# Optimization experiments

Hardware: AMD Instinct MI355X
Metric: run time of the kernel (lower is better)

The kernel has to match this reference:

```python
import jax, jax.numpy as jnp
import numpy as np

N, IN_FEATS, OUT_FEATS = 8192, 512, 256


def setup_inputs() -> dict:
    key = jax.random.key(0)
    k1, k2, k3, k4 = jax.random.split(key, 4)
    feature_mat = jax.random.normal(k1, (N, IN_FEATS), dtype=jnp.float32)
    # Xavier-uniform style init for W and W2
    limW = float(np.sqrt(6.0 / (IN_FEATS + OUT_FEATS)))
    W = jax.random.uniform(k2, (IN_FEATS, OUT_FEATS), minval=-limW, maxval=limW, dtype=jnp.float32)
    limW2 = float(np.sqrt(6.0 / (2 * OUT_FEATS + 1)))
    W2 = jax.random.uniform(k3, (2 * OUT_FEATS, 1), minval=-limW2, maxval=limW2, dtype=jnp.float32)
    adj_mat = jax.random.randint(k4, (N, N), 0, 2, dtype=jnp.int32)
    return {"feature_mat": feature_mat, "W": W, "W2": W2, "adj_mat": adj_mat}


def reference(feature_mat, W, W2, adj_mat):
    out_feats = W.shape[1]
    Wh = feature_mat @ W                      # [N, F']
    Wh1 = Wh @ W2[:out_feats, :]              # [N, 1]
    Wh2 = Wh @ W2[out_feats:, :]              # [N, 1]
    e = Wh1 + Wh2.T                           # [N, N] broadcast add
    e = jnp.where(e > 0, e, 0.2 * e)          # leaky_relu(0.2)
    # NOTE: original masks with ZERO (not -inf) before softmax — faithful.
    e = jnp.where(adj_mat > 0, e, jnp.zeros((), dtype=e.dtype))
    attention = jax.nn.softmax(e, axis=1)     # row softmax over all N
    h_prime = attention @ Wh                  # [N, F']
    return jax.nn.relu(h_prime)
```

## Files before the change

kernel.cpp:

```cpp
#include <hip/hip_runtime.h>
#include <hip/hip_bf16.h>
#include <cstdint>
#include <cstddef>

#define NR 8192
#define FOUT 256
#define KIN 512
#define KSPLIT 4
#define JCHUNK (NR / KSPLIT)
#define BKJ 64
#define NSTEP (JCHUNK / BKJ)
#define IROWS 128

typedef __attribute__((ext_vector_type(8))) short bf16x8;
typedef __attribute__((ext_vector_type(4))) float f32x4;

__device__ __forceinline__ unsigned f2bf(float x) {
  unsigned u = __float_as_uint(x);
  u += 0x7fffu + ((u >> 16) & 1u);
  return u >> 16;
}
__device__ __forceinline__ unsigned f2bf_n(float x) {
  __hip_bfloat16 b = __float2bfloat16(x);
  unsigned short us;
  __builtin_memcpy(&us, &b, 2);
  return (unsigned)us;
}
__device__ __forceinline__ float bf2f_n(unsigned h) {
  unsigned short us = (unsigned short)h;
  __hip_bfloat16 b;
  __builtin_memcpy(&b, &us, 2);
  return __bfloat162float(b);
}
__device__ __forceinline__ unsigned fkey(float x) {
  unsigned u = __float_as_uint(x);
  return (u & 0x80000000u) ? ~u : (u | 0x80000000u);
}
__device__ __forceinline__ float fkey_dec(unsigned k) {
  return __uint_as_float((k & 0x80000000u) ? (k ^ 0x80000000u) : ~k);
}

#define GLDS(g, l)                                                            \
  __builtin_amdgcn_global_load_lds(                                           \
      (const __attribute__((address_space(1))) unsigned int*)(g),             \
      (__attribute__((address_space(3))) unsigned int*)(l), 16, 0, 0)

__global__ __launch_bounds__(256) void k0_prep(const float* __restrict__ W,
                                               const float* __restrict__ W2,
                                               float* __restrict__ w1,
                                               float* __restrict__ w2,
                                               char* __restrict__ WTbf,
                                               unsigned* __restrict__ maxkey) {
  if (blockIdx.x == 0 && threadIdx.x == 0) *maxkey = 0u;
  int wv = threadIdx.x >> 6, lane = threadIdx.x & 63;
  int k = blockIdx.x * 4 + wv;
  int f4 = lane * 4;
  float4 wr = *(const float4*)(W + (size_t)k * FOUT + f4);
  float4 a = *(const float4*)(W2 + f4);
  float4 b = *(const float4*)(W2 + FOUT + f4);
  float d1 = wr.x * a.x + wr.y * a.y + wr.z * a.z + wr.w * a.w;
  float d2 = wr.x * b.x + wr.y * b.y + wr.z * b.z + wr.w * b.w;
#pragma unroll
  for (int off = 32; off; off >>= 1) {
    d1 += __shfl_xor(d1, off);
    d2 += __shfl_xor(d2, off);
  }
  if (lane == 0) {
    w1[k] = d1;
    w2[k] = d2;
  }
  int kt = k >> 5, kl = k & 31;
  float wv4[4] = {wr.x, wr.y, wr.z, wr.w};
#pragma unroll
  for (int ff = 0; ff < 4; ++ff) {
    int f = f4 + ff;
    size_t addr = (size_t)kt * 16384 + (f >> 4) * 1024 +
                  (((f & 15) | (((kl >> 3) & 3) << 4)) * 16) + (kl & 7) * 2;
    *(unsigned short*)(WTbf + addr) = (unsigned short)f2bf(wv4[ff]);
  }
}

__global__ __launch_bounds__(256) void k2_fused(
    const float* __restrict__ X, const char* __restrict__ WTbf,
    const float* __restrict__ w1, const float* __restrict__ w2,
    char* __restrict__ WhTf, float* __restrict__ Wh1, float* __restrict__ Wh2,
    unsigned* __restrict__ maxkey) {
  __shared__ char smem[2 * 18432 + 4096];
  char* buf0 = smem;
  char* buf1 = smem + 18432;
  char* wlds = smem + 2 * 18432;
  int t = threadIdx.x, wv = t >> 6, lane = t & 63;
  int jb = blockIdx.x * 32;
  int jr = t >> 3, koff = (t & 7) * 4;
  int cA = (jr & 15) | (((koff >> 3) & 3) << 4);
  int swA = cA ^ (((cA >> 4) & 3) << 2);
  int aoff = (jr >> 4) * 1024 + swA * 16 + ((koff & 4) << 1);
  int slotR = lane ^ (((lane >> 4) & 3) << 2);
  const float* xrow = X + (size_t)(jb + jr) * KIN + koff;

  {
    float2 a_ = *(const float2*)(w1 + t * 2);
    float2 b_ = *(const float2*)(w2 + t * 2);
    *(float2*)(wlds + t * 8) = a_;
    *(float2*)(wlds + 2048 + t * 8) = b_;
  }
  __syncthreads();

  float4 st0, st1, st2, st3;
  float d1 = 0.f, d2 = 0.f;
  f32x4 acc[2][4];
#pragma unroll
  for (int a = 0; a < 2; ++a)
#pragma unroll
    for (int b = 0; b < 4; ++b) acc[a][b] = (f32x4){0.f, 0.f, 0.f, 0.f};

#define K2_GLB(KT, BUFW)                                                      \
  do {                                                                        \
    const char* gs_ = WTbf + ((size_t)(KT) << 14) + (wv << 12) + lane * 16;   \
    char* ld_ = (BUFW) + 2048 + (wv << 12);                                   \
    GLDS(gs_, ld_);                                                           \
    GLDS(gs_ + 1024, ld_ + 1024);                                             \
    GLDS(gs_ + 2048, ld_ + 2048);                                             \
    GLDS(gs_ + 3072, ld_ + 3072);                                             \
  } while (0)

#define K2_LDX(KT, ST) (ST) = *(const float4*)(xrow + (KT) * 32)

#define K2_AGEN(ST, BUFW, SNUM)                                               \
  do {                                                                        \
    uint2 a_;                                                                 \
    a_.x = f2bf((ST).x) | (f2bf((ST).y) << 16);                               \
    a_.y = f2bf((ST).z) | (f2bf((ST).w) << 16);                               \
    *(uint2*)((BUFW) + aoff) = a_;                                            \
    float4 wa_ = *(const float4*)(wlds + ((SNUM)*32 + koff) * 4);             \
    float4 wb_ = *(const float4*)(wlds + 2048 + ((SNUM)*32 + koff) * 4);      \
    d1 += (ST).x * wa_.x + (ST).y * wa_.y + (ST).z * wa_.z + (ST).w * wa_.w;  \
    d2 += (ST).x * wb_.x + (ST).y * wb_.y + (ST).z * wb_.z + (ST).w * wb_.w;  \
  } while (0)

#define K2_ITER(S, BUFR, BUFW, STC, STF)                                      \
  do {                                                                        \
    int s_ = (S);                                                             \
    if (s_ + 1 < 16) K2_GLB(s_ + 1, BUFW);                                    \
    K2_LDX((s_ + 3 < 16) ? s_ + 3 : 15, STF);                                 \
    if (s_ + 1 < 16) K2_AGEN(STC, BUFW, s_ + 1);                              \
    bf16x8 a0 = *(const bf16x8*)((BUFR) + slotR * 16);                        \
    bf16x8 a1 = *(const bf16x8*)((BUFR) + 1024 + slotR * 16);                 \
    bf16x8 b0 = *(const bf16x8*)((BUFR) + 2048 + (wv * 4 + 0) * 1024 + lane * 16); \
    bf16x8 b1 = *(const bf16x8*)((BUFR) + 2048 + (wv * 4 + 1) * 1024 + lane * 16); \
    bf16x8 b2 = *(const bf16x8*)((BUFR) + 2048 + (wv * 4 + 2) * 1024 + lane * 16); \
    bf16x8 b3 = *(const bf16x8*)((BUFR) + 2048 + (wv * 4 + 3) * 1024 + lane * 16); \
    acc[0][0] = __builtin_amdgcn_mfma_f32_16x16x32_bf16(a0, b0, acc[0][0], 0, 0, 0); \
    acc[0][1] = __builtin_amdgcn_mfma_f32_16x16x32_bf16(a0, b1, acc[0][1], 0, 0, 0); \
    acc[0][2] = __builtin_amdgcn_mfma_f32_16x16x32_bf16(a0, b2, acc[0][2], 0, 0, 0); \
    acc[0][3] = __builtin_amdgcn_mfma_f32_16x16x32_bf16(a0, b3, acc[0][3], 0, 0, 0); \
    acc[1][0] = __builtin_amdgcn_mfma_f32_16x16x32_bf16(a1, b0, acc[1][0], 0, 0, 0); \
    acc[1][1] = __builtin_amdgcn_mfma_f32_16x16x32_bf16(a1, b1, acc[1][1], 0, 0, 0); \
    acc[1][2] = __builtin_amdgcn_mfma_f32_16x16x32_bf16(a1, b2, acc[1][2], 0, 0, 0); \
    acc[1][3] = __builtin_amdgcn_mfma_f32_16x16x32_bf16(a1, b3, acc[1][3], 0, 0, 0); \
    __builtin_amdgcn_sched_barrier(0);                                        \
    asm volatile("s_waitcnt vmcnt(1)");                                       \
    asm volatile("s_waitcnt lgkmcnt(0)");                                     \
    __builtin_amdgcn_s_barrier();                                             \
    __builtin_amdgcn_sched_barrier(0);                                        \
  } while (0)

  K2_GLB(0, buf0);
  K2_LDX(0, st0);
  K2_LDX(1, st1);
  K2_LDX(2, st2);
  K2_AGEN(st0, buf0, 0);
  __builtin_amdgcn_sched_barrier(0);
  asm volatile("s_waitcnt vmcnt(2)");
  asm volatile("s_waitcnt lgkmcnt(0)");
  __builtin_amdgcn_s_barrier();
  __builtin_amdgcn_sched_barrier(0);

  for (int s4 = 0; s4 < 16; s4 += 4) {
    K2_ITER(s4 + 0, buf0, buf1, st1, st3);
    K2_ITER(s4 + 1, buf1, buf0, st2, st0);
    K2_ITER(s4 + 2, buf0, buf1, st3, st1);
    K2_ITER(s4 + 3, buf1, buf0, st0, st2);
  }
#undef K2_ITER
#undef K2_AGEN
#undef K2_LDX
#undef K2_GLB

  int q = lane >> 4;
#pragma unroll
  for (int mi = 0; mi < 2; ++mi)
#pragma unroll
    for (int nn = 0; nn < 4; ++nn) {
      int u2 = wv * 4 + nn;
      int cell = (lane & 15) | ((((mi * 2) + (q >> 1)) & 3) << 4);
      uint2 v;
      v.x = f2bf(acc[mi][nn].x) | (f2bf(acc[mi][nn].y) << 16);
      v.y = f2bf(acc[mi][nn].z) | (f2bf(acc[mi][nn].w) << 16);
      *(uint2*)(buf0 + 2048 + u2 * 1024 + cell * 16 + ((q & 1) << 3)) = v;
    }
  __syncthreads();
  char* wb = WhTf + (size_t)blockIdx.x * 16384;
#pragma unroll
  for (int q2 = 0; q2 < 4; ++q2) {
    uint4 v = *(const uint4*)(buf0 + 2048 + q2 * 4096 + t * 16);
    *(uint4*)(wb + q2 * 4096 + t * 16) = v;
  }

  d1 += __shfl_xor(d1, 1);
  d1 += __shfl_xor(d1, 2);
  d1 += __shfl_xor(d1, 4);
  d2 += __shfl_xor(d2, 1);
  d2 += __shfl_xor(d2, 2);
  d2 += __shfl_xor(d2, 4);
  if ((t & 7) == 0) {
    Wh1[jb + jr] = d1;
    Wh2[jb + jr] = d2;
  }
  float mx = d2;
#pragma unroll
  for (int off = 32; off >= 8; off >>= 1) mx = fmaxf(mx, __shfl_xor(mx, off));
  __shared__ float red[4];
  if (lane == 0) red[wv] = mx;
  __syncthreads();
  if (t == 0) {
    float bm = fmaxf(fmaxf(red[0], red[1]), fmaxf(red[2], red[3]));
    atomicMax(maxkey, fkey(bm));
  }
}

__device__ __forceinline__ uint2 hv4(int4 aq, float4 wq, float wh1, float m,
                                     float enm, float& z) {
  float s0 = wh1 + wq.x, s1 = wh1 + wq.y, s2 = wh1 + wq.z, s3 = wh1 + wq.w;
  s0 = fmaxf(s0, 0.2f * s0);
  s1 = fmaxf(s1, 0.2f * s1);
  s2 = fmaxf(s2, 0.2f * s2);
  s3 = fmaxf(s3, 0.2f * s3);
  float w0 = aq.x > 0 ? __expf(s0 - m) : enm;
  float w1 = aq.y > 0 ? __expf(s1 - m) : enm;
  float w2 = aq.z > 0 ? __expf(s2 - m) : enm;
  float w3 = aq.w > 0 ? __expf(s3 - m) : enm;
  unsigned h0 = f2bf_n(w0), h1 = f2bf_n(w1), h2 = f2bf_n(w2), h3 = f2bf_n(w3);
  z += bf2f_n(h0) + bf2f_n(h1) + bf2f_n(h2) + bf2f_n(h3);
  uint2 r;
  r.x = h0 | (h1 << 16);
  r.y = h2 | (h3 << 16);
  return r;
}
__device__ __forceinline__ uint4 hv8(int4 a0, int4 a1, float4 w0, float4 w1,
                                     float wh1, float m, float enm, float& z) {
  uint2 r0 = hv4(a0, w0, wh1, m, enm, z);
  uint2 r1 = hv4(a1, w1, wh1, m, enm, z);
  return (uint4){r0.x, r0.y, r1.x, r1.y};
}

__global__ __launch_bounds__(1024, 4) void k3_attn(
    const int* __restrict__ adj, const char* __restrict__ WhTf,
    const float* __restrict__ Wh1, const float* __restrict__ Wh2,
    const unsigned* __restrict__ maxptr, float* __restrict__ PVp,
    float* __restrict__ Zp) {
  __shared__ char smem[40960];
  char* abuf0 = smem;
  char* abuf1 = smem + 16384;
  char* wlds = smem + 32768;
  int t = threadIdx.x, wv = t >> 6, lane = t & 63;
  int kc = blockIdx.x & 3;
  int ib = blockIdx.x >> 2;
  int ibase = ib * IROWS;
  int jbch = kc * JCHUNK;
  int r0 = t >> 3;
  int j8 = (t & 7) * 8;
  int iglob = ibase + r0;
  float maxwh2 = fkey_dec(*maxptr);
  float wh1 = Wh1[iglob];
  float m = fmaxf(0.f, wh1 + maxwh2);
  float enm = __expf(-m);
  int unitA = (r0 >> 4) * 2 + (j8 >> 5);
  int cA = (r0 & 15) | (((j8 & 31) >> 3) << 4);
  int swA = cA ^ (((cA >> 4) & 3) << 2);
  int aoff = unitA * 1024 + swA * 16;
  int slotR = lane ^ (((lane >> 4) & 3) << 2);
  const int* adjrow = adj + ((size_t)iglob << 13) + jbch + j8;
  int g = wv >> 1, h = wv & 1;
  const char* bbase = WhTf + ((size_t)(kc * 64) << 14) + (size_t)(2 * g) * 1024 +
                      (size_t)lane * 16;
  const char* wl = wlds + j8 * 4;

  *(float2*)(wlds + t * 8) = *(const float2*)(Wh2 + jbch + t * 2);
  __syncthreads();

  bf16x8 bA00, bA01, bA10, bA11, bB00, bB01, bB10, bB11;
  int4 st0_a, st0_b, st1_a, st1_b;
  f32x4 acc[4][2];
#pragma unroll
  for (int a = 0; a < 4; ++a)
#pragma unroll
    for (int b = 0; b < 2; ++b) acc[a][b] = (f32x4){0.f, 0.f, 0.f, 0.f};
  float zacc = 0.f;

#define K3_LDB(S, B00, B01, B10, B11)                                         \
  do {                                                                        \
    int sc_ = (S) < NSTEP ? (S) : NSTEP - 1;                                  \
    const char* bp_ = bbase + (size_t)(2 * sc_) * 16384;                      \
    B00 = *(const bf16x8*)(bp_);                                 \
    B01 = *(const bf16x8*)(bp_ + 16384);                         \
    B10 = *(const bf16x8*)(bp_ + 1024);                          \
    B11 = *(const bf16x8*)(bp_ + 16384 + 1024);                  \
  } while (0)

#define K3_LDA(S, ST)                                                         \
  do {                                                                        \
    int sc_ = (S) < NSTEP ? (S) : NSTEP - 1;                                  \
    ST##_a = *(const int4*)(adjrow + sc_ * BKJ);                              \
    ST##_b = *(const int4*)(adjrow + sc_ * BKJ + 4);                          \
  } while (0)

#define K3_HV(S, AW, STC)                                                     \
  do {                                                                        \
    float4 wq0_ = *(const float4*)(wl + ((S) + 1) * 256);                     \
    float4 wq1_ = *(const float4*)(wl + ((S) + 1) * 256 + 16);                \
    uint4 a_ = hv8(STC##_a, STC##_b, wq0_, wq1_, wh1, m, enm, zacc);          \
    *(uint4*)((AW) + aoff) = a_;                                              \
  } while (0)

#define K3_MFMA(AR, BC00, BC01, BC10, BC11)                                   \
  do {                                                                        \
    _Pragma("unroll")                                                         \
    for (int rf_ = 0; rf_ < 4; ++rf_) {                                       \
      int ub_ = (h * 4 + rf_) * 2;                                            \
      bf16x8 a0_ = *(const bf16x8*)((AR) + (ub_ + 0) * 1024 + slotR * 16);    \
      bf16x8 a1_ = *(const bf16x8*)((AR) + (ub_ + 1) * 1024 + slotR * 16);    \
      acc[rf_][0] = __builtin_amdgcn_mfma_f32_16x16x32_bf16(a0_, BC00, acc[rf_][0], 0, 0, 0); \
      acc[rf_][1] = __builtin_amdgcn_mfma_f32_16x16x32_bf16(a0_, BC10, acc[rf_][1], 0, 0, 0); \
      acc[rf_][0] = __builtin_amdgcn_mfma_f32_16x16x32_bf16(a1_, BC01, acc[rf_][0], 0, 0, 0); \
      acc[rf_][1] = __builtin_amdgcn_mfma_f32_16x16x32_bf16(a1_, BC11, acc[rf_][1], 0, 0, 0); \
    }                                                                         \
  } while (0)

#define K3_TAIL                                                               \
  do {                                                                        \
    __builtin_amdgcn_sched_barrier(0);                                        \
    asm volatile("s_waitcnt lgkmcnt(0)" ::: "memory");                        \
    __builtin_amdgcn_s_barrier();                                             \
    __builtin_amdgcn_sched_barrier(0);                                        \
  } while (0)

#define K3_ITER_H(S, AR, AW, BC00, BC01, BC10, BC11, BF00, BF01, BF10, BF11,  \
                  STC, DO_HV)                                                 \
  do {                                                                        \
    int s_ = (S);                                                             \
    K3_LDB(s_ + 1, BF00, BF01, BF10, BF11);                                   \
    if (DO_HV) K3_HV(s_, AW, STC);                                            \
    K3_LDA(s_ + 3, STC);                                                      \
    K3_MFMA(AR, BC00, BC01, BC10, BC11);                                      \
    K3_TAIL;                                                                  \
  } while (0)

#define K3_ITER_M(S, AR, AW, BC00, BC01, BC10, BC11, BF00, BF01, BF10, BF11,  \
                  STC, DO_HV)                                                 \
  do {                                                                        \
    int s_ = (S);                                                             \
    K3_LDB(s_ + 1, BF00, BF01, BF10, BF11);                                   \
    K3_MFMA(AR, BC00, BC01, BC10, BC11);                                      \
    if (DO_HV) K3_HV(s_, AW, STC);                                            \
    K3_LDA(s_ + 3, STC);                                                      \
    K3_TAIL;                                                                  \
  } while (0)

  K3_LDB(0, bA00, bA01, bA10, bA11);
  int4 adj0a = *(const int4*)(adjrow);
  int4 adj0b = *(const int4*)(adjrow + 4);
  K3_LDA(1, st1);
  K3_LDA(2, st0);
  {
    float4 wq0 = *(const float4*)(wl);
    float4 wq1 = *(const float4*)(wl + 16);
    uint4 a0 = hv8(adj0a, adj0b, wq0, wq1, wh1, m, enm, zacc);
    *(uint4*)(abuf0 + aoff) = a0;
  }
  K3_TAIL;

  if ((wv & 1) == 0) {
    for (int s2 = 0; s2 < NSTEP - 2; s2 += 2) {
      K3_ITER_H(s2 + 0, abuf0, abuf1, bA00, bA01, bA10, bA11, bB00, bB01,
                bB10, bB11, st1, 1);
      K3_ITER_H(s2 + 1, abuf1, abuf0, bB00, bB01, bB10, bB11, bA00, bA01,
                bA10, bA11, st0, 1);
    }
    K3_ITER_H(NSTEP - 2, abuf0, abuf1, bA00, bA01, bA10, bA11, bB00, bB01,
              bB10, bB11, st1, 1);
    K3_ITER_H(NSTEP - 1, abuf1, abuf0, bB00, bB01, bB10, bB11, bA00, bA01,
              bA10, bA11, st0, 0);
  } else {
    for (int s2 = 0; s2 < NSTEP - 2; s2 += 2) {
      K3_ITER_M(s2 + 0, abuf0, abuf1, bA00, bA01, bA10, bA11, bB00, bB01,
                bB10, bB11, st1, 1);
      K3_ITER_M(s2 + 1, abuf1, abuf0, bB00, bB01, bB10, bB11, bA00, bA01,
                bA10, bA11, st0, 1);
    }
    K3_ITER_M(NSTEP - 2, abuf0, abuf1, bA00, bA01, bA10, bA11, bB00, bB01,
              bB10, bB11, st1, 1);
    K3_ITER_M(NSTEP - 1, abuf1, abuf0, bB00, bB01, bB10, bB11, bA00, bA01,
              bA10, bA11, st0, 0);
  }
#undef K3_ITER_H
#undef K3_ITER_M
#undef K3_TAIL
#undef K3_MFMA
#undef K3_HV
#undef K3_LDA
#undef K3_LDB

  zacc += __shfl_xor(zacc, 1);
  zacc += __shfl_xor(zacc, 2);
  zacc += __shfl_xor(zacc, 4);
  if ((t & 7) == 0) Zp[(size_t)kc * NR + iglob] = zacc;
#pragma unroll
  for (int rf = 0; rf < 4; ++rf)
#pragma unroll
    for (int un = 0; un < 2; ++un) {
      int f = (2 * g + un) * 16 + (lane & 15);
      int row0 = ibase + (h * 4 + rf) * 16 + ((lane >> 4) << 2);
      size_t base = ((size_t)kc * NR + row0) * FOUT + f;
      PVp[base + 0 * FOUT] = acc[rf][un].x;
      PVp[base + 1 * FOUT] = acc[rf][un].y;
      PVp[base + 2 * FOUT] = acc[rf][un].z;
      PVp[base + 3 * FOUT] = acc[rf][un].w;
    }
}

__global__ __launch_bounds__(256) void k4_reduce(const float* __restrict__ PVp,
                                                 const float* __restrict__ Zp,
                                                 float* __restrict__ out) {
  int tid = blockIdx.x * 256 + threadIdx.x;
  int i = tid >> 6;
  int f4 = (tid & 63) * 4;
  float z = Zp[i] + Zp[NR + i] + Zp[2 * NR + i] + Zp[3 * NR + i];
  float4 a = {0.f, 0.f, 0.f, 0.f};
#pragma unroll
  for (int c = 0; c < KSPLIT; ++c) {
    float4 p = *(const float4*)(PVp + ((size_t)c * NR + i) * FOUT + f4);
    a.x += p.x;
    a.y += p.y;
    a.z += p.z;
    a.w += p.w;
  }
  float inv = 1.f / z;
  float4 r;
  r.x = fmaxf(a.x * inv, 0.f);
  r.y = fmaxf(a.y * inv, 0.f);
  r.z = fmaxf(a.z * inv, 0.f);
  r.w = fmaxf(a.w * inv, 0.f);
  *(float4*)(out + (size_t)i * FOUT + f4) = r;
}

extern "C" void kernel_launch(void* const* d_in, const int* in_sizes, int n_in,
                              void* d_out, int out_size, void* d_ws,
                              size_t ws_size, hipStream_t stream) {
  const float* X = (const float*)d_in[0];
  const float* W = (const float*)d_in[1];
  const float* W2 = (const float*)d_in[2];
  const int* adj = (const int*)d_in[3];
  float* out = (float*)d_out;
  char* ws = (char*)d_ws;

  const size_t WHT_OFF = 0;
  const size_t WTBF_OFF = (size_t)4 * 1024 * 1024;
  const size_t W1_OFF = WTBF_OFF + 256 * 1024;
  const size_t W2V_OFF = W1_OFF + 2048;
  const size_t WH1_OFF = W2V_OFF + 2048;
  const size_t WH2_OFF = WH1_OFF + 32768;
  const size_t MXK_OFF = WH2_OFF + 32768;
  const size_t ZP_OFF = MXK_OFF + 256;
  const size_t PV_OFF = ZP_OFF + (size_t)KSPLIT * NR * 4;

  char* WhTf = ws + WHT_OFF;
  char* WTbf = ws + WTBF_OFF;
  float* w1 = (float*)(ws + W1_OFF);
  float* w2 = (float*)(ws + W2V_OFF);
  float* Wh1 = (float*)(ws + WH1_OFF);
  float* Wh2 = (float*)(ws + WH2_OFF);
  unsigned* maxkey = (unsigned*)(ws + MXK_OFF);
  float* Zp = (float*)(ws + ZP_OFF);
  float* PVp = (float*)(ws + PV_OFF);

  k0_prep<<<128, 256, 0, stream>>>(W, W2, w1, w2, WTbf, maxkey);
  k2_fused<<<256, 256, 0, stream>>>(X, WTbf, w1, w2, WhTf, Wh1, Wh2, maxkey);
  k3_attn<<<256, 1024, 0, stream>>>(adj, WhTf, Wh1, Wh2, maxkey, PVp, Zp);
  k4_reduce<<<2048, 256, 0, stream>>>(PVp, Zp, out);
}
```

Measured before the change: 106.9 us.

## Process two K-steps per barrier window with four rotating LDS attention buffers

```diff
diff --git a/kernel.cpp b/kernel.cpp
--- a/kernel.cpp
+++ b/kernel.cpp
@@ -259,10 +259,9 @@
     const float* __restrict__ Wh1, const float* __restrict__ Wh2,
     const unsigned* __restrict__ maxptr, float* __restrict__ PVp,
     float* __restrict__ Zp) {
-  __shared__ char smem[40960];
-  char* abuf0 = smem;
-  char* abuf1 = smem + 16384;
-  char* wlds = smem + 32768;
+  __shared__ char smem[73728];
+  char* ab[4] = {smem, smem + 16384, smem + 32768, smem + 49152};
+  char* wlds = smem + 65536;
   int t = threadIdx.x, wv = t >> 6, lane = t & 63;
   int kc = blockIdx.x & 3;
   int ib = blockIdx.x >> 2;
@@ -289,8 +288,8 @@
   *(float2*)(wlds + t * 8) = *(const float2*)(Wh2 + jbch + t * 2);
   __syncthreads();
 
-  bf16x8 bA00, bA01, bA10, bA11, bB00, bB01, bB10, bB11;
-  int4 st0_a, st0_b, st1_a, st1_b;
+  bf16x8 p00, p01, p10, p11, q00, q01, q10, q11;
+  int4 stC_a, stC_b, stD_a, stD_b;
   f32x4 acc[4][2];
 #pragma unroll
   for (int a = 0; a < 4; ++a)
@@ -315,11 +314,11 @@
     ST##_b = *(const int4*)(adjrow + sc_ * BKJ + 4);                          \
   } while (0)
 
-#define K3_HV(S, AW, STC)                                                     \
-  do {                                                                        \
-    float4 wq0_ = *(const float4*)(wl + ((S) + 1) * 256);                     \
-    float4 wq1_ = *(const float4*)(wl + ((S) + 1) * 256 + 16);                \
-    uint4 a_ = hv8(STC##_a, STC##_b, wq0_, wq1_, wh1, m, enm, zacc);          \
+#define K3_HVG(SS, AW, ST)                                                    \
+  do {                                                                        \
+    float4 wq0_ = *(const float4*)(wl + (SS) * 256);                          \
+    float4 wq1_ = *(const float4*)(wl + (SS) * 256 + 16);                     \
+    uint4 a_ = hv8(ST##_a, ST##_b, wq0_, wq1_, wh1, m, enm, zacc);            \
     *(uint4*)((AW) + aoff) = a_;                                              \
   } while (0)
 
@@ -345,69 +344,74 @@
     __builtin_amdgcn_sched_barrier(0);                                        \
   } while (0)
 
-#define K3_ITER_H(S, AR, AW, BC00, BC01, BC10, BC11, BF00, BF01, BF10, BF11,  \
-                  STC, DO_HV)                                                 \
-  do {                                                                        \
-    int s_ = (S);                                                             \
-    K3_LDB(s_ + 1, BF00, BF01, BF10, BF11);                                   \
-    if (DO_HV) K3_HV(s_, AW, STC);                                            \
-    K3_LDA(s_ + 3, STC);                                                      \
-    K3_MFMA(AR, BC00, BC01, BC10, BC11);                                      \
+#define K3_WIN_H(S, PR0, PR1, PW0, PW1, DO_HV)                                \
+  do {                                                                        \
+    K3_LDB((S), p00, p01, p10, p11);                                          \
+    K3_LDB((S) + 1, q00, q01, q10, q11);                                      \
+    if (DO_HV) {                                                              \
+      K3_HVG((S) + 2, PW0, stC);                                              \
+      K3_HVG((S) + 3, PW1, stD);                                              \
+    }                                                                         \
+    K3_LDA((S) + 4, stC);                                                     \
+    K3_LDA((S) + 5, stD);                                                     \
+    K3_MFMA(PR0, p00, p01, p10, p11);                                         \
+    K3_MFMA(PR1, q00, q01, q10, q11);                                         \
     K3_TAIL;                                                                  \
   } while (0)
 
-#define K3_ITER_M(S, AR, AW, BC00, BC01, BC10, BC11, BF00, BF01, BF10, BF11,  \
-                  STC, DO_HV)                                                 \
-  do {                                                                        \
-    int s_ = (S);                                                             \
-    K3_LDB(s_ + 1, BF00, BF01, BF10, BF11);                                   \
-    K3_MFMA(AR, BC00, BC01, BC10, BC11);                                      \
-    if (DO_HV) K3_HV(s_, AW, STC);                                            \
-    K3_LDA(s_ + 3, STC);                                                      \
+#define K3_WIN_M(S, PR0, PR1, PW0, PW1, DO_HV)                                \
+  do {                                                                        \
+    K3_LDB((S), p00, p01, p10, p11);                                          \
+    K3_LDB((S) + 1, q00, q01, q10, q11);                                      \
+    K3_MFMA(PR0, p00, p01, p10, p11);                                         \
+    K3_MFMA(PR1, q00, q01, q10, q11);                                         \
+    if (DO_HV) {                                                              \
+      K3_HVG((S) + 2, PW0, stC);                                              \
+      K3_HVG((S) + 3, PW1, stD);                                              \
+    }                                                                         \
+    K3_LDA((S) + 4, stC);                                                     \
+    K3_LDA((S) + 5, stD);                                                     \
     K3_TAIL;                                                                  \
   } while (0)
 
-  K3_LDB(0, bA00, bA01, bA10, bA11);
-  int4 adj0a = *(const int4*)(adjrow);
-  int4 adj0b = *(const int4*)(adjrow + 4);
-  K3_LDA(1, st1);
-  K3_LDA(2, st0);
   {
+    int4 a0a = *(const int4*)(adjrow);
+    int4 a0b = *(const int4*)(adjrow + 4);
+    int4 a1a = *(const int4*)(adjrow + BKJ);
+    int4 a1b = *(const int4*)(adjrow + BKJ + 4);
+    K3_LDA(2, stC);
+    K3_LDA(3, stD);
     float4 wq0 = *(const float4*)(wl);
     float4 wq1 = *(const float4*)(wl + 16);
-    uint4 a0 = hv8(adj0a, adj0b, wq0, wq1, wh1, m, enm, zacc);
-    *(uint4*)(abuf0 + aoff) = a0;
+    uint4 av0 = hv8(a0a, a0b, wq0, wq1, wh1, m, enm, zacc);
+    *(uint4*)(ab[0] + aoff) = av0;
+    float4 wq2 = *(const float4*)(wl + 256);
+    float4 wq3 = *(const float4*)(wl + 256 + 16);
+    uint4 av1 = hv8(a1a, a1b, wq2, wq3, wh1, m, enm, zacc);
+    *(uint4*)(ab[1] + aoff) = av1;
   }
   K3_TAIL;
 
   if ((wv & 1) == 0) {
-    for (int s2 = 0; s2 < NSTEP - 2; s2 += 2) {
-      K3_ITER_H(s2 + 0, abuf0, abuf1, bA00, bA01, bA10, bA11, bB00, bB01,
-                bB10, bB11, st1, 1);
-      K3_ITER_H(s2 + 1, abuf1, abuf0, bB00, bB01, bB10, bB11, bA00, bA01,
-                bA10, bA11, st0, 1);
+    for (int s4 = 0; s4 < NSTEP - 4; s4 += 4) {
+      K3_WIN_H(s4 + 0, ab[0], ab[1], ab[2], ab[3], 1);
+      K3_WIN_H(s4 + 2, ab[2], ab[3], ab[0], ab[1], 1);
     }
-    K3_ITER_H(NSTEP - 2, abuf0, abuf1, bA00, bA01, bA10, bA11, bB00, bB01,
-              bB10, bB11, st1, 1);
-    K3_ITER_H(NSTEP - 1, abuf1, abuf0, bB00, bB01, bB10, bB11, bA00, bA01,
-              bA10, bA11, st0, 0);
+    K3_WIN_H(NSTEP - 4, ab[0], ab[1], ab[2], ab[3], 1);
+    K3_WIN_H(NSTEP - 2, ab[2], ab[3], ab[0], ab[1], 0);
   } else {
-    for (int s2 = 0; s2 < NSTEP - 2; s2 += 2) {
-      K3_ITER_M(s2 + 0, abuf0, abuf1, bA00, bA01, bA10, bA11, bB00, bB01,
-                bB10, bB11, st1, 1);
-      K3_ITER_M(s2 + 1, abuf1, abuf0, bB00, bB01, bB10, bB11, bA00, bA01,
-                bA10, bA11, st0, 1);
+    for (int s4 = 0; s4 < NSTEP - 4; s4 += 4) {
+      K3_WIN_M(s4 + 0, ab[0], ab[1], ab[2], ab[3], 1);
+      K3_WIN_M(s4 + 2, ab[2], ab[3], ab[0], ab[1], 1);
     }
-    K3_ITER_M(NSTEP - 2, abuf0, abuf1, bA00, bA01, bA10, bA11, bB00, bB01,
-              bB10, bB11, st1, 1);
-    K3_ITER_M(NSTEP - 1, abuf1, abuf0, bB00, bB01, bB10, bB11, bA00, bA01,
-              bA10, bA11, st0, 0);
-  }
-#undef K3_ITER_H
-#undef K3_ITER_M
+    K3_WIN_M(NSTEP - 4, ab[0], ab[1], ab[2], ab[3], 1);
+    K3_WIN_M(NSTEP - 2, ab[2], ab[3], ab[0], ab[1], 0);
+  }
+#undef K3_WIN_H
+#undef K3_WIN_M
 #undef K3_TAIL
 #undef K3_MFMA
-#undef K3_HV
+#undef K3_HVG
 #undef K3_LDA
 #undef K3_LDB
 
```

After: 109.8 us. 1.03x slower.
